# Kernel tuning notes

Measured on AMD Instinct MI355X. Metric: run time of the kernel, lower is better.

## Reference

```python
import jax, jax.numpy as jnp
import numpy as np

LAYERS, DIM, FFN, HEADS = 2, 1024, 4096, 8
HD = DIM // HEADS          # head qk dim = 128
VD = DIM                   # v_dim (double_v_dim=False)
HV = VD // HEADS           # head v dim = 128
B, L = 2, 2048
SCALE_BASE = 512.0
EPS = 1e-5


def setup_inputs() -> dict:
    key = jax.random.key(0)
    ks = jax.random.split(key, 18)
    def rn(k, shape, s=1.0):
        return jax.random.normal(k, shape, dtype=jnp.float32) * s
    return dict(
        X=rn(ks[0], (B, L, DIM)),
        Wq=rn(ks[1], (LAYERS, HEADS, DIM, HD), 1.0 / DIM),
        Wk=rn(ks[2], (LAYERS, HEADS, DIM, HD), 1.0 / DIM),
        Wv=rn(ks[3], (LAYERS, HEADS, DIM, HV), 1.0 / DIM),
        W_G=rn(ks[4], (LAYERS, DIM, VD), 1.0 / DIM),
        W_O=rn(ks[5], (LAYERS, VD, DIM), 1.0 / DIM),
        gn_w=1.0 + 0.02 * rn(ks[6], (LAYERS, VD)),
        gn_b=0.02 * rn(ks[7], (LAYERS, VD)),
        ln1_w=1.0 + 0.02 * rn(ks[8], (LAYERS, DIM)),
        ln1_b=0.02 * rn(ks[9], (LAYERS, DIM)),
        ln2_w=1.0 + 0.02 * rn(ks[10], (LAYERS, DIM)),
        ln2_b=0.02 * rn(ks[11], (LAYERS, DIM)),
        ffn_w1=rn(ks[12], (LAYERS, DIM, FFN), DIM ** -0.5),
        ffn_b1=0.02 * rn(ks[13], (LAYERS, FFN)),
        ffn_w2=rn(ks[14], (LAYERS, FFN, DIM), FFN ** -0.5),
        ffn_b2=0.02 * rn(ks[15], (LAYERS, DIM)),
    )


def _xpos_tables(length, head_dim):
    half = head_dim // 2
    pos = jnp.arange(length, dtype=jnp.float32)
    base_scale = (jnp.arange(0, head_dim, 2, dtype=jnp.float32) + 0.4 * head_dim) / (1.4 * head_dim)
    sc = base_scale[None, :] ** (pos / SCALE_BASE)[:, None]          # [L, half]
    inv_freq = 1.0 / (10000.0 ** (jnp.arange(half, dtype=jnp.float32) / half))
    ang = pos[:, None] * inv_freq[None, :]                           # [L, half]
    return sc, jnp.sin(ang), jnp.cos(ang)


def _dup(t):
    # duplicate_interleave: [L, half] -> [L, head_dim]
    return jnp.repeat(t, 2, axis=-1)


def _rotate_every_two(x):
    x1, x2 = x[..., ::2], x[..., 1::2]
    return jnp.stack([-x2, x1], axis=-1).reshape(x.shape)


def _apply_xpos(x, sc, sin, cos, downscale):
    s = 1.0 / sc if downscale else sc
    return x * _dup(cos * s) + _rotate_every_two(x) * _dup(sin * s)


def _layernorm(x, w, b):
    mu = jnp.mean(x, axis=-1, keepdims=True)
    var = jnp.var(x, axis=-1, keepdims=True)
    return (x - mu) * jax.lax.rsqrt(var + EPS) * w + b


def _decay_matrix(length):
    gammas = jnp.asarray(1.0 - np.exp(np.linspace(np.log(1 / 32), np.log(1 / 512), HEADS)), dtype=jnp.float32)
    n = jnp.arange(length, dtype=jnp.float32)
    delta = n[:, None] - n[None, :]                                  # [L, L]
    logg = jnp.log(gammas)[:, None, None]                            # [H, 1, 1]
    return jnp.where(delta[None] >= 0, jnp.exp(logg * delta[None]), 0.0)  # [H, L, L]


def _msr(X, Wq, Wk, Wv, gn_w, gn_b, W_G, W_O, D, sc, sin, cos):
    b, l, d = X.shape
    Q = _apply_xpos(jnp.einsum('bld,hde->bhle', X, Wq), sc, sin, cos, False)
    K = _apply_xpos(jnp.einsum('bld,hde->bhle', X, Wk), sc, sin, cos, True)
    V = jnp.einsum('bld,hdv->bhlv', X, Wv)
    scores = jnp.einsum('bhle,bhme->bhlm', Q, K) * D[None]           # [B,H,L,L] decayed
    Y = jnp.einsum('bhlm,bhmv->bhlv', scores, V)                     # [B,H,L,HV]
    # GroupNorm(heads, v_dim) over per-token concatenated heads == per-head norm
    mu = jnp.mean(Y, axis=-1, keepdims=True)
    var = jnp.var(Y, axis=-1, keepdims=True)
    Yn = (Y - mu) * jax.lax.rsqrt(var + EPS)
    Yn = Yn * gn_w.reshape(HEADS, 1, HV)[None] + gn_b.reshape(HEADS, 1, HV)[None]
    Yc = jnp.transpose(Yn, (0, 2, 1, 3)).reshape(b, l, VD)
    G = X @ W_G
    gate = G * jax.nn.sigmoid(G)                                     # swish
    return (gate * Yc) @ W_O


def reference(X, Wq, Wk, Wv, W_G, W_O, gn_w, gn_b, ln1_w, ln1_b, ln2_w, ln2_b, ffn_w1, ffn_b1, ffn_w2, ffn_b2):
    l = X.shape[1]
    sc, sin, cos = _xpos_tables(l, HD)
    D = _decay_matrix(l)
    for i in range(LAYERS):
        Y = _msr(_layernorm(X, ln1_w[i], ln1_b[i]), Wq[i], Wk[i], Wv[i],
                 gn_w[i], gn_b[i], W_G[i], W_O[i], D, sc, sin, cos) + X
        h = _layernorm(Y, ln2_w[i], ln2_b[i])
        h = jax.nn.gelu(h @ ffn_w1[i] + ffn_b1[i], approximate=False)
        X = h @ ffn_w2[i] + ffn_b2[i] + Y                            # Dropout is identity in eval
    return X
```

## Files before the change

kernel.cpp:

```cpp
#include <hip/hip_runtime.h>
#include <math.h>

#define DIM 1024
#define FFN_DIM 4096
#define HEADS 8
#define HD 128
#define BB 2
#define LL 2048
#define NROWS (BB*LL)

typedef __attribute__((ext_vector_type(8))) short bf16x8;
typedef __attribute__((ext_vector_type(4))) short bf16x4;
typedef __attribute__((ext_vector_type(2))) short bf16x2;
typedef __attribute__((ext_vector_type(4))) float f32x4;

__device__ inline short f2bf(float f) {
    unsigned u = __builtin_bit_cast(unsigned, f);
    unsigned r = (u + 0x7FFFu + ((u >> 16) & 1u)) >> 16;
    return (short)r;
}
__device__ inline float bf2f(short s) {
    unsigned u = ((unsigned)(unsigned short)s) << 16;
    return __builtin_bit_cast(float, u);
}

__device__ __forceinline__ void gl_lds16(const void* g, void* l) {
    __builtin_amdgcn_global_load_lds(
        (const __attribute__((address_space(1))) unsigned int*)g,
        (__attribute__((address_space(3))) unsigned int*)l, 16, 0, 0);
}

__global__ __launch_bounds__(256) void ln_kernel_bf(
    const float* __restrict__ x, const float* __restrict__ w,
    const float* __restrict__ b, short* __restrict__ out)
{
    int row = blockIdx.x;
    int tid = threadIdx.x;
    const float* xr = x + (size_t)row * DIM;
    float4 v = *(const float4*)(xr + tid * 4);
    float s  = v.x + v.y + v.z + v.w;
    float ss = v.x*v.x + v.y*v.y + v.z*v.z + v.w*v.w;
    #pragma unroll
    for (int o = 32; o > 0; o >>= 1) { s += __shfl_down(s, o); ss += __shfl_down(ss, o); }
    __shared__ float red[10];
    int wid = tid >> 6;
    if ((tid & 63) == 0) { red[wid] = s; red[4 + wid] = ss; }
    __syncthreads();
    if (tid == 0) {
        float t  = red[0] + red[1] + red[2] + red[3];
        float t2 = red[4] + red[5] + red[6] + red[7];
        float mu  = t * (1.f / DIM);
        float var = t2 * (1.f / DIM) - mu * mu;
        red[8] = mu; red[9] = rsqrtf(var + 1e-5f);
    }
    __syncthreads();
    float mu = red[8], rs = red[9];
    float4 wv = *(const float4*)(w + tid * 4);
    float4 bv = *(const float4*)(b + tid * 4);
    bf16x4 o;
    o[0] = f2bf((v.x - mu) * rs * wv.x + bv.x);
    o[1] = f2bf((v.y - mu) * rs * wv.y + bv.y);
    o[2] = f2bf((v.z - mu) * rs * wv.z + bv.z);
    o[3] = f2bf((v.w - mu) * rs * wv.w + bv.w);
    *(bf16x4*)(out + (size_t)row * DIM + tid * 4) = o;
}

__global__ __launch_bounds__(256) void transpose_cvt(
    const float* __restrict__ in, short* __restrict__ out,
    int R, int C, size_t ibs, size_t obs)
{
    __shared__ float t[32][33];
    int bz = blockIdx.z;
    int r0 = blockIdx.y * 32, c0 = blockIdx.x * 32;
    int tx = threadIdx.x & 31, ty = threadIdx.x >> 5;
    const float* ip = in + (size_t)bz * ibs;
    short* op = out + (size_t)bz * obs;
    #pragma unroll
    for (int i = 0; i < 4; ++i)
        t[ty + i * 8][tx] = ip[(size_t)(r0 + ty + i * 8) * C + c0 + tx];
    __syncthreads();
    #pragma unroll
    for (int i = 0; i < 4; ++i)
        op[(size_t)(c0 + ty + i * 8) * R + r0 + tx] = f2bf(t[tx][ty + i * 8]);
}

__global__ __launch_bounds__(256) void vt_cvt(
    const short* __restrict__ Vb, short* __restrict__ Vt)
{
    __shared__ short t[32][34];
    int r0 = blockIdx.y * 32, c0 = blockIdx.x * 32;
    int tx = threadIdx.x & 31, ty = threadIdx.x >> 5;
    #pragma unroll
    for (int i = 0; i < 4; ++i)
        t[ty + i * 8][tx] = Vb[(size_t)(r0 + ty + i * 8) * DIM + c0 + tx];
    __syncthreads();
    int b = r0 >> 11;
    int l = (r0 & (LL - 1));
    #pragma unroll
    for (int i = 0; i < 4; ++i) {
        int c = c0 + ty + i * 8;
        int h = c >> 7, v = c & 127;
        Vt[(((size_t)(b * HEADS + h) * HD + v) << 11) + l + tx] = t[tx][ty + i * 8];
    }
}

template<int EPI, int MI, int NI, int GX>
__global__ __launch_bounds__(512, 2) void gemm_pipe(
    const short* __restrict__ A, const short* __restrict__ Bt,
    void* __restrict__ Cv, const float* __restrict__ bias,
    const float* __restrict__ R_,
    void* __restrict__ P1, void* __restrict__ P2, void* __restrict__ P3,
    int N, int K, int M)
{
    constexpr int BM = 32 * MI;
    constexpr int BN = 64 * NI;
    constexpr int LA = BM / 64;
    constexpr int LB = BN / 64;
    __shared__ __align__(16) short As[2][BM * 64];
    __shared__ __align__(16) short Bs[2][BN * 64];
    int tid = threadIdx.x;
    int w = tid >> 6, lane = tid & 63;
    int q = lane >> 4, lr = lane & 15;
    int wr = w >> 2, wc = w & 3;

    int id = blockIdx.y * GX + blockIdx.x;
    int xcd = id & 7, j = id >> 3;
    constexpr int rx_n = (GX >= 8) ? GX / 8 : 1;
    int tp = (GX * gridDim.y) >> 3;
    int rh = tp >> 3;
    int lbx = j & 7, lby = j >> 3;
    int rx = xcd % rx_n, ry = xcd / rx_n;
    int bm = (ry * rh + lby) * BM;
    int bn = (rx * 8 + lbx) * BN;

    int srow = tid >> 3;
    int sseg = tid & 7;

    f32x4 acc[MI][NI];
    #pragma unroll
    for (int mi = 0; mi < MI; ++mi)
        #pragma unroll
        for (int ni = 0; ni < NI; ++ni) acc[mi][ni] = (f32x4){0.f, 0.f, 0.f, 0.f};

    auto stageA = [&](int bb, int k0) {
        #pragma unroll
        for (int i = 0; i < LA; ++i) {
            int row = i * 64 + srow;
            gl_lds16(A + (size_t)(bm + row) * K + k0 + ((sseg ^ (row & 7)) << 3),
                     &As[bb][(i * 512 + tid) * 8]);
        }
    };
    auto stageB = [&](int bb, int k0) {
        #pragma unroll
        for (int i = 0; i < LB; ++i) {
            int row = i * 64 + srow;
            gl_lds16(Bt + (size_t)(bn + row) * K + k0 + ((sseg ^ (row & 7)) << 3),
                     &Bs[bb][(i * 512 + tid) * 8]);
        }
    };

    stageA(0, 0);
    stageB(0, 0);

    int aoff = (wr * (BM / 2) + lr) * 64;
    int boff = (wc * (BN / 4) + lr) * 64;
    int seg0 = ((q ^ (lr & 7)) << 3);
    int seg1 = (((4 + q) ^ (lr & 7)) << 3);

    int nk = K >> 6;
    #pragma unroll 1
    for (int kt = 0; kt < nk; ++kt) {
        int b = kt & 1;
        if (kt + 1 < nk) {
            stageA(b ^ 1, (kt + 1) << 6);
            if constexpr (LA == 4)
                asm volatile("s_waitcnt vmcnt(4)\ns_barrier" ::: "memory");
            else
                asm volatile("s_waitcnt vmcnt(2)\ns_barrier" ::: "memory");
        } else {
            asm volatile("s_waitcnt vmcnt(0)\ns_barrier" ::: "memory");
        }
        const short* as = As[b];
        const short* bs = Bs[b];
        bf16x8 af[MI], bfr[NI];
        #pragma unroll
        for (int mi = 0; mi < MI; ++mi)
            af[mi] = *(const bf16x8*)&as[aoff + mi * 1024 + seg0];
        #pragma unroll
        for (int ni = 0; ni < NI; ++ni)
            bfr[ni] = *(const bf16x8*)&bs[boff + ni * 1024 + seg0];
        __builtin_amdgcn_s_setprio(1);
        #pragma unroll
        for (int mi = 0; mi < MI; ++mi)
            #pragma unroll
            for (int ni = 0; ni < NI; ++ni)
                acc[mi][ni] = __builtin_amdgcn_mfma_f32_16x16x32_bf16(af[mi], bfr[ni], acc[mi][ni], 0, 0, 0);
        __builtin_amdgcn_s_setprio(0);
        if (kt + 1 < nk) stageB(b ^ 1, (kt + 1) << 6);
        #pragma unroll
        for (int mi = 0; mi < MI; ++mi)
            af[mi] = *(const bf16x8*)&as[aoff + mi * 1024 + seg1];
        #pragma unroll
        for (int ni = 0; ni < NI; ++ni)
            bfr[ni] = *(const bf16x8*)&bs[boff + ni * 1024 + seg1];
        __builtin_amdgcn_s_setprio(1);
        #pragma unroll
        for (int mi = 0; mi < MI; ++mi)
            #pragma unroll
            for (int ni = 0; ni < NI; ++ni)
                acc[mi][ni] = __builtin_amdgcn_mfma_f32_16x16x32_bf16(af[mi], bfr[ni], acc[mi][ni], 0, 0, 0);
        __builtin_amdgcn_s_setprio(0);
        asm volatile("s_barrier" ::: "memory");
    }

    if constexpr (EPI == 4) {
        int sel = bn >> 10;
        int row_base = bm + wr * (BM / 2) + q * 4;
        int l0 = row_base & (LL - 1);
        #pragma unroll
        for (int ni = 0; ni < NI; ++ni) {
            int col = bn + wc * (BN / 4) + ni * 16 + lr;
            int cq = col & (DIM - 1);
            if (sel <= 1) {
                int jj = (col & 127) >> 1;
                float lb = log2f((2.f * jj + 51.2f) / 179.2f);
                if (sel == 1) lb = -lb;
                float invf = exp2f(-(float)jj * (13.287712379549449f / 64.f));
                float snb, cnb;
                sincosf((float)l0 * invf, &snb, &cnb);
                float scb = exp2f(lb * (float)l0 * (1.f / 512.f));
                float s1, c1, s16, c16;
                __sincosf(invf, &s1, &c1);
                __sincosf(16.f * invf, &s16, &c16);
                float st1 = exp2f(lb * (1.f / 512.f));
                float st16 = exp2f(lb * (16.f / 512.f));
                short* Ob = (short*)(sel == 0 ? Cv : P1);
                #pragma unroll
                for (int mi = 0; mi < MI; ++mi) {
                    float cr = cnb, sr = snb, sv = scb;
                    #pragma unroll
                    for (int r = 0; r < 4; ++r) {
                        float cs = cr * sv, ssn = sr * sv;
                        float v = acc[mi][ni][r];
                        float p = __shfl_xor(v, 1);
                        float o = (lr & 1) ? (v * cs + p * ssn) : (v * cs - p * ssn);
                        Ob[(size_t)(row_base + mi * 16 + r) * DIM + cq] = f2bf(o);
                        if (r < 3) {
                            float crn = cr * c1 - sr * s1;
                            sr = sr * c1 + cr * s1; cr = crn;
                            sv *= st1;
                        }
                    }
                    float cbn = cnb * c16 - snb * s16;
                    snb = snb * c16 + cnb * s16; cnb = cbn;
                    scb *= st16;
                }
            } else if (sel == 2) {
                short* Vb = (short*)P2;
                #pragma unroll
                for (int mi = 0; mi < MI; ++mi)
                    #pragma unroll
                    for (int r = 0; r < 4; ++r)
                        Vb[(size_t)(row_base + mi * 16 + r) * DIM + cq] = f2bf(acc[mi][ni][r]);
            } else {
                short* Gb = (short*)P3;
                #pragma unroll
                for (int mi = 0; mi < MI; ++mi)
                    #pragma unroll
                    for (int r = 0; r < 4; ++r)
                        Gb[(size_t)(row_base + mi * 16 + r) * DIM + cq] = f2bf(acc[mi][ni][r]);
            }
        }
        return;
    }

    float* Cf = (float*)Cv;
    short* Cs = (short*)Cv;
    #pragma unroll
    for (int ni = 0; ni < NI; ++ni) {
        int col = bn + wc * (BN / 4) + ni * 16 + lr;
        float bi = 0.f;
        if constexpr (EPI == 1 || EPI == 2) bi = bias[col];
        #pragma unroll
        for (int mi = 0; mi < MI; ++mi) {
            int row0 = bm + wr * (BM / 2) + mi * 16 + q * 4;
            #pragma unroll
            for (int r = 0; r < 4; ++r) {
                size_t off = (size_t)(row0 + r) * M + col;
                float v = acc[mi][ni][r];
                if constexpr (EPI == 1) {
                    v += bi;
                    v = 0.5f * v * (1.f + erff(v * 0.70710678118654752f));
                    Cs[off] = f2bf(v);
                } else if constexpr (EPI == 2) {
                    Cf[off] = v + bi + R_[off];
                } else if constexpr (EPI == 3) {
                    Cf[off] = v + R_[off];
                } else {
                    Cf[off] = v;
                }
            }
        }
    }
}

#define PSTR 40
__global__ __launch_bounds__(256) void retention_mfma2(
    const short* __restrict__ Qb, const short* __restrict__ Kb,
    const short* __restrict__ Vt, float* __restrict__ Y)
{
    __shared__ __align__(16) short Ks[2][32 * 128];
    __shared__ __align__(16) short Vs[2][128 * 32];
    __shared__ __align__(16) short Ps[4][16 * PSTR];
    int tid = threadIdx.x;
    int w = tid >> 6, lane = tid & 63;
    int q = lane >> 4, lr = lane & 15;
    int bh = blockIdx.x;
    int b = bh >> 3, h = bh & 7;
    size_t bL = (size_t)b * LL;
    const short* Kbh = Kb + (bL << 10) + (h << 7);
    const short* Qbh = Qb + (bL << 10) + (h << 7);
    const short* Vbh = Vt + ((size_t)bh << 18);
    float* Ybh = Y + (bL << 10) + (h << 7);

    const float lg_lo = -3.4657359027997265f;
    const float lg_hi = -6.2383246250395075f;
    float gamma = 1.f - expf(lg_lo + (lg_hi - lg_lo) * ((float)h / 7.f));
    float logg = logf(gamma);
    float gm32 = expf(-32.f * logg);
    float rf[4];
    #pragma unroll
    for (int r = 0; r < 4; ++r) rf[r] = expf(logg * (float)(q * 4 + r));
    float cf0 = expf(-logg * (float)lr);
    float cf1 = expf(-logg * (float)(16 + lr));
    int dqlr = q * 4 - lr;

    int krow = lane >> 4;
    int kslot = lane & 15;
    int vrow = lane >> 2;
    int vslot = lane & 3;

    #pragma unroll 1
    for (int pass = 0; pass < 2; ++pass) {
        int jt = pass ? (31 - blockIdx.y) : blockIdx.y;
        int l0w = jt * 64 + w * 16;
        int ntiles = 2 * jt + 2;

        bf16x8 qf[4];
        {
            const short* qp = Qbh + ((size_t)(l0w + lr) << 10) + q * 8;
            #pragma unroll
            for (int es = 0; es < 4; ++es) qf[es] = *(const bf16x8*)(qp + es * 32);
        }
        f32x4 yacc[8];
        #pragma unroll
        for (int vt = 0; vt < 8; ++vt) yacc[vt] = (f32x4){0.f, 0.f, 0.f, 0.f};
        float tf = expf(logg * (float)l0w);

        #pragma unroll
        for (int i = 0; i < 2; ++i) {
            int kr = w * 8 + i * 4 + krow;
            gl_lds16(Kbh + ((size_t)kr << 10) + ((kslot ^ (kr & 15)) << 3),
                     &Ks[0][(w * 8 + i * 4) * 128]);
            int vr = w * 32 + i * 16 + vrow;
            gl_lds16(Vbh + ((size_t)vr << 11) + ((vslot ^ (vr & 3)) << 3),
                     &Vs[0][(w * 32 + i * 16) * 32]);
        }

        #pragma unroll 1
        for (int mt = 0; mt < ntiles; ++mt) {
            int cur = mt & 1;
            int m0 = mt * 32;
            __syncthreads();
            if (mt + 1 < ntiles) {
                int m1 = m0 + 32;
                #pragma unroll
                for (int i = 0; i < 2; ++i) {
                    int kr = w * 8 + i * 4 + krow;
                    gl_lds16(Kbh + ((size_t)(m1 + kr) << 10) + ((kslot ^ (kr & 15)) << 3),
                             &Ks[cur ^ 1][(w * 8 + i * 4) * 128]);
                    int vr = w * 32 + i * 16 + vrow;
                    gl_lds16(Vbh + ((size_t)vr << 11) + m1 + ((vslot ^ (vr & 3)) << 3),
                             &Vs[cur ^ 1][(w * 32 + i * 16) * 32]);
                }
            }
            if (m0 <= l0w + 15) {
                int dt = l0w - m0;
                f32x4 sa0 = (f32x4){0.f,0.f,0.f,0.f};
                f32x4 sa1 = (f32x4){0.f,0.f,0.f,0.f};
                #pragma unroll
                for (int es = 0; es < 4; ++es) {
                    int slot = ((es * 4 + q) ^ lr) * 8;
                    bf16x8 bk0 = *(const bf16x8*)&Ks[cur][lr * 128 + slot];
                    bf16x8 bk1 = *(const bf16x8*)&Ks[cur][(16 + lr) * 128 + slot];
                    sa0 = __builtin_amdgcn_mfma_f32_16x16x32_bf16(qf[es], bk0, sa0, 0, 0, 0);
                    sa1 = __builtin_amdgcn_mfma_f32_16x16x32_bf16(qf[es], bk1, sa1, 0, 0, 0);
                }
                #pragma unroll
                for (int r = 0; r < 4; ++r) {
                    float p0 = sa0[r] * (rf[r] * cf0 * tf);
                    float p1 = sa1[r] * (rf[r] * cf1 * tf);
                    int d0 = dt + dqlr + r;
                    Ps[w][(q*4 + r) * PSTR + lr]      = (d0 >= 0)      ? f2bf(p0) : (short)0;
                    Ps[w][(q*4 + r) * PSTR + 16 + lr] = (d0 - 16 >= 0) ? f2bf(p1) : (short)0;
                }
                bf16x8 pa = *(const bf16x8*)&Ps[w][lr * PSTR + q * 8];
                int vslot_r = (q ^ (lr & 3)) * 8;
                #pragma unroll
                for (int vt = 0; vt < 8; ++vt) {
                    bf16x8 bv = *(const bf16x8*)&Vs[cur][(vt * 16 + lr) * 32 + vslot_r];
                    yacc[vt] = __builtin_amdgcn_mfma_f32_16x16x32_bf16(pa, bv, yacc[vt], 0, 0, 0);
                }
            }
            tf *= gm32;
        }
        __syncthreads();
        float* yp = Ybh + ((size_t)(l0w + q * 4) << 10) + lr;
        #pragma unroll
        for (int vt = 0; vt < 8; ++vt)
            #pragma unroll
            for (int r = 0; r < 4; ++r)
                yp[((size_t)r << 10) + vt * 16] = yacc[vt][r];
    }
}

__global__ __launch_bounds__(256) void gn_gate_kernel(
    const float* __restrict__ Y, const short* __restrict__ Gb,
    const float* __restrict__ w, const float* __restrict__ b,
    short* __restrict__ ybf)
{
    int tid = threadIdx.x;
    int wid = tid >> 6, lane = tid & 63;
    int grp = blockIdx.x * 4 + wid;
    int n = grp >> 3, h = grp & 7;
    size_t base = (size_t)n * DIM + h * HD + lane * 2;
    float2 y = *(const float2*)(Y + base);
    float s = y.x + y.y, ss = y.x * y.x + y.y * y.y;
    #pragma unroll
    for (int o = 32; o > 0; o >>= 1) { s += __shfl_down(s, o); ss += __shfl_down(ss, o); }
    s = __shfl(s, 0); ss = __shfl(ss, 0);
    float mu  = s * (1.f / HD);
    float var = ss * (1.f / HD) - mu * mu;
    float rs  = rsqrtf(var + 1e-5f);
    float2 wv = *(const float2*)(w + h * HD + lane * 2);
    float2 bv = *(const float2*)(b + h * HD + lane * 2);
    bf16x2 gv = *(const bf16x2*)(Gb + base);
    float gx = bf2f(gv[0]), gy = bf2f(gv[1]);
    float g0 = gx / (1.f + expf(-gx));
    float g1 = gy / (1.f + expf(-gy));
    bf16x2 o;
    o[0] = f2bf(((y.x - mu) * rs * wv.x + bv.x) * g0);
    o[1] = f2bf(((y.y - mu) * rs * wv.y + bv.y) * g1);
    *(bf16x2*)(ybf + base) = o;
}

extern "C" void kernel_launch(void* const* d_in, const int* in_sizes, int n_in,
                              void* d_out, int out_size, void* d_ws, size_t ws_size,
                              hipStream_t stream)
{
    const float* X0   = (const float*)d_in[0];
    const float* Wq   = (const float*)d_in[1];
    const float* Wk   = (const float*)d_in[2];
    const float* Wv   = (const float*)d_in[3];
    const float* WG   = (const float*)d_in[4];
    const float* WO   = (const float*)d_in[5];
    const float* gnw  = (const float*)d_in[6];
    const float* gnb  = (const float*)d_in[7];
    const float* ln1w = (const float*)d_in[8];
    const float* ln1b = (const float*)d_in[9];
    const float* ln2w = (const float*)d_in[10];
    const float* ln2b = (const float*)d_in[11];
    const float* fw1  = (const float*)d_in[12];
    const float* fb1  = (const float*)d_in[13];
    const float* fw2  = (const float*)d_in[14];
    const float* fb2  = (const float*)d_in[15];

    float* ws = (float*)d_ws;
    const size_t U = (size_t)NROWS * DIM;

    short* lnbf  = (short*)(ws + 0 * U);
    short* wqkvg = lnbf + (size_t)NROWS * DIM;
    short* Vt   = (short*)(ws + 1 * U);
    short* fw1t = (short*)(ws + 1 * U);
    short* fw2t = fw1t + (size_t)DIM * FFN_DIM;
    float* sY  = ws + 2 * U;
    short* h1   = (short*)(ws + 2 * U);
    short* Vb   = (short*)(ws + 3 * U);
    short* ybf  = (short*)(ws + 3 * U);
    short* wot  = ybf + (size_t)NROWS * DIM;
    short* Gb   = (short*)(ws + 4 * U);
    float* sXn = ws + 4 * U;
    short* Qb   = (short*)(ws + 5 * U);
    short* Kb   = Qb + (size_t)NROWS * DIM;
    float* sX  = ws + 6 * U;

    for (int i = 0; i < 2; ++i) {
        const float* Xin = (i == 0) ? X0 : sX;
        float* Xout = (i == 1) ? (float*)d_out : sX;

        ln_kernel_bf<<<NROWS, 256, 0, stream>>>(Xin, ln1w + i * DIM, ln1b + i * DIM, lnbf);
        dim3 tq(HD / 32, DIM / 32, HEADS);
        transpose_cvt<<<tq, 256, 0, stream>>>(Wq + (size_t)i * HEADS * DIM * HD, wqkvg + 0 * DIM * DIM, DIM, HD, (size_t)DIM * HD, (size_t)HD * DIM);
        transpose_cvt<<<tq, 256, 0, stream>>>(Wk + (size_t)i * HEADS * DIM * HD, wqkvg + 1 * DIM * DIM, DIM, HD, (size_t)DIM * HD, (size_t)HD * DIM);
        transpose_cvt<<<tq, 256, 0, stream>>>(Wv + (size_t)i * HEADS * DIM * HD, wqkvg + 2 * DIM * DIM, DIM, HD, (size_t)DIM * HD, (size_t)HD * DIM);
        dim3 tg(DIM / 32, DIM / 32, 1);
        transpose_cvt<<<tg, 256, 0, stream>>>(WG + (size_t)i * DIM * DIM, wqkvg + 3 * (size_t)DIM * DIM, DIM, DIM, 0, 0);
        dim3 gp4(4 * DIM / 256, NROWS / 256);
        gemm_pipe<4, 8, 4, 16><<<gp4, 512, 0, stream>>>(lnbf, wqkvg, Qb, nullptr, nullptr, Kb, Vb, Gb, NROWS, DIM, 4 * DIM);
        dim3 vg(DIM / 32, NROWS / 32);
        vt_cvt<<<vg, 256, 0, stream>>>(Vb, Vt);
        dim3 rg(16, 16);
        retention_mfma2<<<rg, 256, 0, stream>>>(Qb, Kb, Vt, sY);
        gn_gate_kernel<<<NROWS * HEADS / 4, 256, 0, stream>>>(sY, Gb, gnw + i * DIM, gnb + i * DIM, ybf);
        transpose_cvt<<<tg, 256, 0, stream>>>(WO + (size_t)i * DIM * DIM, wot, DIM, DIM, 0, 0);
        dim3 gp(DIM / 128, NROWS / 128);
        gemm_pipe<3, 4, 2, 8><<<gp, 512, 0, stream>>>(ybf, wot, sXn, nullptr, Xin, nullptr, nullptr, nullptr, NROWS, DIM, DIM);
        ln_kernel_bf<<<NROWS, 256, 0, stream>>>(sXn, ln2w + i * DIM, ln2b + i * DIM, lnbf);
        dim3 t1(FFN_DIM / 32, DIM / 32, 1);
        transpose_cvt<<<t1, 256, 0, stream>>>(fw1 + (size_t)i * DIM * FFN_DIM, fw1t, DIM, FFN_DIM, 0, 0);
        dim3 t2(DIM / 32, FFN_DIM / 32, 1);
        transpose_cvt<<<t2, 256, 0, stream>>>(fw2 + (size_t)i * FFN_DIM * DIM, fw2t, FFN_DIM, DIM, 0, 0);
        dim3 gf1(FFN_DIM / 256, NROWS / 256);
        gemm_pipe<1, 8, 4, 16><<<gf1, 512, 0, stream>>>(lnbf, fw1t, h1, fb1 + i * FFN_DIM, nullptr, nullptr, nullptr, nullptr, NROWS, DIM, FFN_DIM);
        dim3 gf2(DIM / 128, NROWS / 128);
        gemm_pipe<2, 4, 2, 8><<<gf2, 512, 0, stream>>>(h1, fw2t, Xout, fb2 + i * DIM, sXn, nullptr, nullptr, nullptr, NROWS, FFN_DIM, DIM);
    }
}
```

Measured before the change: 799.6 us.

## Split retention key range across two wave groups with LDS reduction

The retention kernel now runs 512 threads per block. Two groups of four waves each process alternate 32-key halves of a 64-key stage, and their partial outputs are reduced through shared memory at the end. The K/V staging tile doubles to 64 keys and uses manual vmcnt waits plus raw barriers in place of a full syncthreads. The goal is more waves in flight per block and fewer barriers per key, at the cost of extra LDS, an added reduction step, and idle work on masked causal halves.

```diff
diff --git a/kernel.cpp b/kernel.cpp
--- a/kernel.cpp
+++ b/kernel.cpp
@@ -305,16 +305,18 @@
 }
 
 #define PSTR 40
-__global__ __launch_bounds__(256) void retention_mfma2(
+__global__ __launch_bounds__(512, 2) void retention_mfma2(
     const short* __restrict__ Qb, const short* __restrict__ Kb,
     const short* __restrict__ Vt, float* __restrict__ Y)
 {
-    __shared__ __align__(16) short Ks[2][32 * 128];
-    __shared__ __align__(16) short Vs[2][128 * 32];
-    __shared__ __align__(16) short Ps[4][16 * PSTR];
+    __shared__ __align__(16) short Ks[2][64 * 128];
+    __shared__ __align__(16) short Vs[2][128 * 64];
+    __shared__ __align__(16) short Ps[8][16 * PSTR];
     int tid = threadIdx.x;
     int w = tid >> 6, lane = tid & 63;
     int q = lane >> 4, lr = lane & 15;
+    int g = w >> 2;
+    int qw = w & 3;
     int bh = blockIdx.x;
     int b = bh >> 3, h = bh & 7;
     size_t bL = (size_t)b * LL;
@@ -327,7 +329,7 @@
     const float lg_hi = -6.2383246250395075f;
     float gamma = 1.f - expf(lg_lo + (lg_hi - lg_lo) * ((float)h / 7.f));
     float logg = logf(gamma);
-    float gm32 = expf(-32.f * logg);
+    float gm64 = expf(-64.f * logg);
     float rf[4];
     #pragma unroll
     for (int r = 0; r < 4; ++r) rf[r] = expf(logg * (float)(q * 4 + r));
@@ -335,16 +337,29 @@
     float cf1 = expf(-logg * (float)(16 + lr));
     int dqlr = q * 4 - lr;
 
-    int krow = lane >> 4;
-    int kslot = lane & 15;
-    int vrow = lane >> 2;
-    int vslot = lane & 3;
+    int kr_l = lane >> 4;
+    int ks_l = lane & 15;
+    int vr_l = lane >> 3;
+    int vs_l = lane & 7;
+
+    auto stageKV = [&](int bb, int m0) {
+        #pragma unroll
+        for (int i = 0; i < 2; ++i) {
+            int ch = w * 2 + i;
+            int kr = ch * 4 + kr_l;
+            gl_lds16(Kbh + ((size_t)(m0 + kr) << 10) + ((ks_l ^ (kr & 15)) << 3),
+                     &Ks[bb][ch * 512]);
+            int vr = ch * 8 + vr_l;
+            gl_lds16(Vbh + ((size_t)vr << 11) + m0 + ((vs_l ^ (vr & 7)) << 3),
+                     &Vs[bb][ch * 512]);
+        }
+    };
 
     #pragma unroll 1
     for (int pass = 0; pass < 2; ++pass) {
         int jt = pass ? (31 - blockIdx.y) : blockIdx.y;
-        int l0w = jt * 64 + w * 16;
-        int ntiles = 2 * jt + 2;
+        int l0w = jt * 64 + qw * 16;
+        int ns = jt + 1;
 
         bf16x8 qf[4];
         {
@@ -355,44 +370,30 @@
         f32x4 yacc[8];
         #pragma unroll
         for (int vt = 0; vt < 8; ++vt) yacc[vt] = (f32x4){0.f, 0.f, 0.f, 0.f};
-        float tf = expf(logg * (float)l0w);
-
-        #pragma unroll
-        for (int i = 0; i < 2; ++i) {
-            int kr = w * 8 + i * 4 + krow;
-            gl_lds16(Kbh + ((size_t)kr << 10) + ((kslot ^ (kr & 15)) << 3),
-                     &Ks[0][(w * 8 + i * 4) * 128]);
-            int vr = w * 32 + i * 16 + vrow;
-            gl_lds16(Vbh + ((size_t)vr << 11) + ((vslot ^ (vr & 3)) << 3),
-                     &Vs[0][(w * 32 + i * 16) * 32]);
-        }
+        float tf = expf(logg * (float)(l0w - g * 32));
+
+        stageKV(0, 0);
 
         #pragma unroll 1
-        for (int mt = 0; mt < ntiles; ++mt) {
-            int cur = mt & 1;
-            int m0 = mt * 32;
-            __syncthreads();
-            if (mt + 1 < ntiles) {
-                int m1 = m0 + 32;
-                #pragma unroll
-                for (int i = 0; i < 2; ++i) {
-                    int kr = w * 8 + i * 4 + krow;
-                    gl_lds16(Kbh + ((size_t)(m1 + kr) << 10) + ((kslot ^ (kr & 15)) << 3),
-                             &Ks[cur ^ 1][(w * 8 + i * 4) * 128]);
-                    int vr = w * 32 + i * 16 + vrow;
-                    gl_lds16(Vbh + ((size_t)vr << 11) + m1 + ((vslot ^ (vr & 3)) << 3),
-                             &Vs[cur ^ 1][(w * 32 + i * 16) * 32]);
-                }
+        for (int s = 0; s < ns; ++s) {
+            int buf = s & 1;
+            if (s + 1 < ns) {
+                stageKV(buf ^ 1, (s + 1) * 64);
+                asm volatile("s_waitcnt vmcnt(4)\ns_barrier" ::: "memory");
+            } else {
+                asm volatile("s_waitcnt vmcnt(0)\ns_barrier" ::: "memory");
             }
+            int m0 = s * 64 + g * 32;
             if (m0 <= l0w + 15) {
                 int dt = l0w - m0;
+                const short* ksub = &Ks[buf][g * 32 * 128];
                 f32x4 sa0 = (f32x4){0.f,0.f,0.f,0.f};
                 f32x4 sa1 = (f32x4){0.f,0.f,0.f,0.f};
                 #pragma unroll
                 for (int es = 0; es < 4; ++es) {
                     int slot = ((es * 4 + q) ^ lr) * 8;
-                    bf16x8 bk0 = *(const bf16x8*)&Ks[cur][lr * 128 + slot];
-                    bf16x8 bk1 = *(const bf16x8*)&Ks[cur][(16 + lr) * 128 + slot];
+                    bf16x8 bk0 = *(const bf16x8*)&ksub[lr * 128 + slot];
+                    bf16x8 bk1 = *(const bf16x8*)&ksub[(16 + lr) * 128 + slot];
                     sa0 = __builtin_amdgcn_mfma_f32_16x16x32_bf16(qf[es], bk0, sa0, 0, 0, 0);
                     sa1 = __builtin_amdgcn_mfma_f32_16x16x32_bf16(qf[es], bk1, sa1, 0, 0, 0);
                 }
@@ -405,22 +406,35 @@
                     Ps[w][(q*4 + r) * PSTR + 16 + lr] = (d0 - 16 >= 0) ? f2bf(p1) : (short)0;
                 }
                 bf16x8 pa = *(const bf16x8*)&Ps[w][lr * PSTR + q * 8];
-                int vslot_r = (q ^ (lr & 3)) * 8;
                 #pragma unroll
                 for (int vt = 0; vt < 8; ++vt) {
-                    bf16x8 bv = *(const bf16x8*)&Vs[cur][(vt * 16 + lr) * 32 + vslot_r];
+                    bf16x8 bv = *(const bf16x8*)&Vs[buf][(vt * 16 + lr) * 64 + (((g * 4 + q) ^ (lr & 7)) << 3)];
                     yacc[vt] = __builtin_amdgcn_mfma_f32_16x16x32_bf16(pa, bv, yacc[vt], 0, 0, 0);
                 }
             }
-            tf *= gm32;
+            tf *= gm64;
+            asm volatile("s_barrier" ::: "memory");
         }
         __syncthreads();
-        float* yp = Ybh + ((size_t)(l0w + q * 4) << 10) + lr;
-        #pragma unroll
-        for (int vt = 0; vt < 8; ++vt)
+        float* sc = (float*)&Ks[0][0] + qw * 2048;
+        if (g) {
             #pragma unroll
-            for (int r = 0; r < 4; ++r)
-                yp[((size_t)r << 10) + vt * 16] = yacc[vt][r];
+            for (int vt = 0; vt < 8; ++vt)
+                #pragma unroll
+                for (int r = 0; r < 4; ++r)
+                    sc[(q * 4 + r) * 128 + ((vt * 16 + lr) ^ (q * 8))] = yacc[vt][r];
+        }
+        __syncthreads();
+        if (!g) {
+            float* yp = Ybh + ((size_t)(l0w + q * 4) << 10) + lr;
+            #pragma unroll
+            for (int vt = 0; vt < 8; ++vt)
+                #pragma unroll
+                for (int r = 0; r < 4; ++r)
+                    yp[((size_t)r << 10) + vt * 16] =
+                        yacc[vt][r] + sc[(q * 4 + r) * 128 + ((vt * 16 + lr) ^ (q * 8))];
+        }
+        __syncthreads();
     }
 }
 
@@ -510,7 +524,7 @@
         dim3 vg(DIM / 32, NROWS / 32);
         vt_cvt<<<vg, 256, 0, stream>>>(Vb, Vt);
         dim3 rg(16, 16);
-        retention_mfma2<<<rg, 256, 0, stream>>>(Qb, Kb, Vt, sY);
+        retention_mfma2<<<rg, 512, 0, stream>>>(Qb, Kb, Vt, sY);
         gn_gate_kernel<<<NROWS * HEADS / 4, 256, 0, stream>>>(sY, Gb, gnw + i * DIM, gnb + i * DIM, ybf);
         transpose_cvt<<<tg, 256, 0, stream>>>(WO + (size_t)i * DIM * DIM, wot, DIM, DIM, 0, 0);
         dim3 gp(DIM / 128, NROWS / 128);
```

New measurement: 747.4 us. 1.07x faster.
